# Optimization experiments

Measured on AMD Instinct MI355X. Metric: run time of the kernel, lower is better.

The kernel has to match this reference:

```python
import jax, jax.numpy as jnp
import numpy as np

B, S, F = 2, 2048, 1024
H, D = 16, 64
INIT = 0.02


def setup_inputs() -> dict:
    key = jax.random.key(0)
    k1, k2, k3 = jax.random.split(key, 3)
    x = jax.random.normal(k1, (B, S, F), dtype=jnp.float32)
    w_attn = jax.random.normal(k2, (F, 3 * F), dtype=jnp.float32) * INIT
    b_attn = jnp.zeros((3 * F,), dtype=jnp.float32)
    w_proj = jax.random.normal(k3, (F, F), dtype=jnp.float32) * INIT
    b_proj = jnp.zeros((F,), dtype=jnp.float32)
    return {"x": x, "w_attn": w_attn, "b_attn": b_attn, "w_proj": w_proj, "b_proj": b_proj}


def reference(x, w_attn, b_attn, w_proj, b_proj):
    # c_attn: [..., S, F] -> [..., S, 3F]
    qkv = jnp.einsum('bsf,fe->bse', x, w_attn) + b_attn
    q, k, v = jnp.split(qkv, 3, axis=-1)
    # split heads: [..., S, F] -> [..., S, H, D]
    q = q.reshape(q.shape[:-1] + (H, D))
    k = k.reshape(k.shape[:-1] + (H, D))
    v = v.reshape(v.shape[:-1] + (H, D))
    q = q / jnp.sqrt(jnp.asarray(D, dtype=q.dtype))
    # scores: [..., H, Sq, Sk]
    scores = jnp.einsum('bqhd,bkhd->bhqk', q, k)
    seq = x.shape[-2]
    causal = jnp.tril(jnp.ones((seq, seq), dtype=bool))  # [Sq, Sk]
    big_neg = jnp.finfo(scores.dtype).min
    scores = jnp.where(causal, scores, big_neg)
    weights = jax.nn.softmax(scores, axis=-1)
    z = jnp.einsum('bhqk,bkhd->bqhd', weights, v)
    merged = z.reshape(z.shape[:-2] + (F,))
    out = jnp.einsum('bsf,fe->bse', merged, w_proj) + b_proj
    return out
```

## Files before the change

### kernel.cpp

```cpp
#include <hip/hip_runtime.h>

#define B_ 2
#define S_ 2048
#define F_ 1024
#define H_ 16
#define D_ 64

typedef __bf16 bf16x8 __attribute__((ext_vector_type(8)));
typedef float f32x4 __attribute__((ext_vector_type(4)));
typedef float f32x16 __attribute__((ext_vector_type(16)));

union U8 { unsigned int u[4]; bf16x8 v; };

__device__ __forceinline__ unsigned short f2bf(float f) {
    union { float f; unsigned int u; } v;
    v.f = f;
    unsigned int r = v.u + 0x7fffu + ((v.u >> 16) & 1u);
    return (unsigned short)(r >> 16);
}

__device__ __forceinline__ unsigned int cvtpk_bf16(float lo, float hi) {
    unsigned int r;
    asm("v_cvt_pk_bf16_f32 %0, %1, %2" : "=v"(r) : "v"(lo), "v"(hi));
    return r;
}

__device__ __forceinline__ float xhalf_sum(float x) {
    return x + __shfl_xor(x, 32);
}

__device__ __forceinline__ void gload16(const unsigned short* g, unsigned short* l) {
    __builtin_amdgcn_global_load_lds(
        (const __attribute__((address_space(1))) unsigned int*)g,
        (__attribute__((address_space(3))) unsigned int*)l,
        16, 0, 0);
}

__global__ __launch_bounds__(256) void prep_kernel(const float* __restrict__ x, unsigned short* __restrict__ xb,
                                                   const float* __restrict__ wa, unsigned short* __restrict__ wat,
                                                   const float* __restrict__ wp, unsigned short* __restrict__ wpt) {
    __shared__ float t[32][33];
    int bid = blockIdx.x, tid = threadIdx.x;
    if (bid < 4096) {
        int i = bid * 256 + tid;
        float4 v = reinterpret_cast<const float4*>(x)[i];
        ushort4 o;
        o.x = f2bf(v.x); o.y = f2bf(v.y); o.z = f2bf(v.z); o.w = f2bf(v.w);
        reinterpret_cast<ushort4*>(xb)[i] = o;
        return;
    }
    const float* in;
    unsigned short* out;
    int R, C, bx, by;
    if (bid < 7168) {
        int loc = bid - 4096;
        bx = loc % 96; by = loc / 96;
        in = wa; out = wat; R = 1024; C = 3072;
    } else {
        int loc = bid - 7168;
        bx = loc & 31; by = loc >> 5;
        in = wp; out = wpt; R = 1024; C = 1024;
    }
    int tx = tid & 31, ty = tid >> 5;
    int r0 = by << 5, c0 = bx << 5;
#pragma unroll
    for (int kk = 0; kk < 4; ++kk)
        t[ty + 8 * kk][tx] = in[(size_t)(r0 + ty + 8 * kk) * C + c0 + tx];
    __syncthreads();
#pragma unroll
    for (int kk = 0; kk < 4; ++kk)
        out[(size_t)(c0 + ty + 8 * kk) * R + r0 + tx] = f2bf(t[tx][ty + 8 * kk]);
}

__global__ __launch_bounds__(512, 2) void gemm_qkv(const unsigned short* __restrict__ A,
                                                   const unsigned short* __restrict__ Bt,
                                                   const float* __restrict__ bias,
                                                   unsigned short* __restrict__ qo,
                                                   unsigned short* __restrict__ ko,
                                                   unsigned short* __restrict__ vo) {
    __shared__ __align__(16) unsigned short lds[65536];
    const int K = 1024;
    int bid = blockIdx.x;
    int swz = (bid & 7) * 24 + (bid >> 3);
    int by = swz / 12, bx = swz % 12;
    int m0 = by << 8, n0 = bx << 8;
    int tid = threadIdx.x;
    int wid = tid >> 6, l = tid & 63, lg = l >> 4, lr = l & 15;
    int wr = wid >> 2, wc = wid & 3;
    f32x4 acc[8][4] = {};

    int g0 = tid, g1 = tid + 512;
    int r0 = g0 >> 3, p0 = g0 & 7;
    int r1 = g1 >> 3, p1 = g1 & 7;
    int c0 = (p0 ^ (r0 & 7)) << 3;
    int c1 = (p1 ^ (r1 & 7)) << 3;

    int xr = (lr & 7) << 3;
    int csw0 = (lg * 8) ^ xr;
    int csw1 = (32 + lg * 8) ^ xr;

    const unsigned short* A0 = A + (size_t)(m0 + r0) * K + c0;
    const unsigned short* A1 = A + (size_t)(m0 + r1) * K + c1;
    const unsigned short* A2 = A + (size_t)(m0 + 128 + r0) * K + c0;
    const unsigned short* A3 = A + (size_t)(m0 + 128 + r1) * K + c1;
    const unsigned short* B0 = Bt + (size_t)(n0 + r0) * K + c0;
    const unsigned short* B1 = Bt + (size_t)(n0 + r1) * K + c1;
    const unsigned short* B2 = Bt + (size_t)(n0 + 128 + r0) * K + c0;
    const unsigned short* B3 = Bt + (size_t)(n0 + 128 + r1) * K + c1;

    gload16(A0, &lds[g0 * 8]);
    gload16(A1, &lds[g1 * 8]);
    gload16(A2, &lds[8192 + g0 * 8]);
    gload16(A3, &lds[8192 + g1 * 8]);
    gload16(B0, &lds[16384 + g0 * 8]);
    gload16(B1, &lds[16384 + g1 * 8]);
    gload16(B2, &lds[24576 + g0 * 8]);
    gload16(B3, &lds[24576 + g1 * 8]);
    __syncthreads();

    for (int t = 0; t < 16; ++t) {
        int bo = (t & 1) * 32768;
        if (t < 15) {
            int no = ((t + 1) & 1) * 32768;
            int t64 = (t + 1) * 64;
            gload16(A0 + t64, &lds[no + g0 * 8]);
            gload16(A1 + t64, &lds[no + g1 * 8]);
            gload16(A2 + t64, &lds[no + 8192 + g0 * 8]);
            gload16(A3 + t64, &lds[no + 8192 + g1 * 8]);
            gload16(B0 + t64, &lds[no + 16384 + g0 * 8]);
            gload16(B1 + t64, &lds[no + 16384 + g1 * 8]);
            gload16(B2 + t64, &lds[no + 24576 + g0 * 8]);
            gload16(B3 + t64, &lds[no + 24576 + g1 * 8]);
        }
        bf16x8 Bf[8];
#pragma unroll
        for (int ni = 0; ni < 4; ++ni) {
            int rowB = wc * 64 + ni * 16 + lr;
            int ba = bo + 16384 + (rowB >> 7) * 8192 + (rowB & 127) * 64;
            Bf[ni * 2]     = *reinterpret_cast<const bf16x8*>(&lds[ba + csw0]);
            Bf[ni * 2 + 1] = *reinterpret_cast<const bf16x8*>(&lds[ba + csw1]);
        }
#pragma unroll
        for (int mi = 0; mi < 8; ++mi) {
            int aa = bo + wr * 8192 + (mi * 16 + lr) * 64;
            bf16x8 a0 = *reinterpret_cast<const bf16x8*>(&lds[aa + csw0]);
            bf16x8 a1 = *reinterpret_cast<const bf16x8*>(&lds[aa + csw1]);
#pragma unroll
            for (int ni = 0; ni < 4; ++ni) {
                acc[mi][ni] = __builtin_amdgcn_mfma_f32_16x16x32_bf16(a0, Bf[ni * 2], acc[mi][ni], 0, 0, 0);
                acc[mi][ni] = __builtin_amdgcn_mfma_f32_16x16x32_bf16(a1, Bf[ni * 2 + 1], acc[mi][ni], 0, 0, 0);
            }
        }
        __syncthreads();
    }

#pragma unroll
    for (int mi = 0; mi < 8; ++mi) {
#pragma unroll
        for (int ni = 0; ni < 4; ++ni) {
            int col = n0 + wc * 64 + ni * 16 + lr;
            float bv = bias[col];
            int part = col >> 10, cc = col & 1023, h = cc >> 6, d = cc & 63;
            int row0 = m0 + wr * 128 + mi * 16 + (lg << 2);
            int bb = row0 >> 11, s0 = row0 & 2047;
            int bh = bb * H_ + h;
            if (part == 2) {
                int jt = s0 >> 5, db = d >> 5, kf2 = (s0 >> 4) & 1, hi2 = (s0 >> 3) & 1;
                int ll = (d & 31) | (hi2 << 5), e0 = s0 & 7;
                ushort4 pk;
                unsigned short* p = reinterpret_cast<unsigned short*>(&pk);
#pragma unroll
                for (int r = 0; r < 4; ++r) p[r] = f2bf(acc[mi][ni][r] + bv);
                *reinterpret_cast<ushort4*>(
                    &vo[(size_t)((((bh * 64 + jt) * 2 + db) * 2 + kf2)) * 512 + ll * 8 + e0]) = pk;
            } else {
                unsigned short* dst = part == 0 ? qo : ko;
                float scale = part == 0 ? 0.125f * 1.44269504f : 1.0f;
                int t2 = s0 >> 5, kf2 = d >> 4, e = d & 7;
                int lbase = ((d >> 3) & 1) << 5;
                size_t fb = (size_t)((bh * 64 + t2) * 4 + kf2) * 512 + e;
#pragma unroll
                for (int r = 0; r < 4; ++r) {
                    float vv = (acc[mi][ni][r] + bv) * scale;
                    dst[fb + (size_t)((((s0 + r) & 31) | lbase)) * 8] = f2bf(vv);
                }
            }
        }
    }
}

__global__ __launch_bounds__(256) void gemm_proj(const unsigned short* __restrict__ A,
                                                 const unsigned short* __restrict__ Bt,
                                                 const float* __restrict__ bias,
                                                 float* __restrict__ out) {
    __shared__ __align__(16) unsigned short As[2 * 128 * 32];
    __shared__ __align__(16) unsigned short Bs[2 * 128 * 32];
    const int K = 1024, NT = 32;
    int m0 = blockIdx.y << 7, n0 = blockIdx.x << 7;
    int tid = threadIdx.x;
    int w = tid >> 6, l = tid & 63, lg = l >> 4, lr = l & 15;
    int wm = (w >> 1) << 6, wn = (w & 1) << 6;
    f32x4 acc[4][4] = {};

    int sr = tid >> 2, sc = (tid & 3) << 3;
    const unsigned short* Ab = A + (size_t)(m0 + sr) * K + sc;
    const unsigned short* Bb = Bt + (size_t)(n0 + sr) * K + sc;
    const size_t half = (size_t)64 * K;

    gload16(Ab, &As[tid * 8]);
    gload16(Ab + half, &As[2048 + tid * 8]);
    gload16(Bb, &Bs[tid * 8]);
    gload16(Bb + half, &Bs[2048 + tid * 8]);
    __syncthreads();

    for (int t = 0; t < NT; ++t) {
        int cur = (t & 1) * 4096;
        if (t + 1 < NT) {
            int nxt = ((t + 1) & 1) * 4096;
            int ko2 = (t + 1) * 32;
            gload16(Ab + ko2, &As[nxt + tid * 8]);
            gload16(Ab + ko2 + half, &As[nxt + 2048 + tid * 8]);
            gload16(Bb + ko2, &Bs[nxt + tid * 8]);
            gload16(Bb + ko2 + half, &Bs[nxt + 2048 + tid * 8]);
        }
        bf16x8 af[4], bfr[4];
#pragma unroll
        for (int mi = 0; mi < 4; ++mi)
            af[mi] = *reinterpret_cast<const bf16x8*>(&As[cur + (wm + mi * 16 + lr) * 32 + (lg << 3)]);
#pragma unroll
        for (int ni = 0; ni < 4; ++ni)
            bfr[ni] = *reinterpret_cast<const bf16x8*>(&Bs[cur + (wn + ni * 16 + lr) * 32 + (lg << 3)]);
#pragma unroll
        for (int mi = 0; mi < 4; ++mi)
#pragma unroll
            for (int ni = 0; ni < 4; ++ni)
                acc[mi][ni] = __builtin_amdgcn_mfma_f32_16x16x32_bf16(af[mi], bfr[ni], acc[mi][ni], 0, 0, 0);
        __syncthreads();
    }
#pragma unroll
    for (int mi = 0; mi < 4; ++mi) {
#pragma unroll
        for (int ni = 0; ni < 4; ++ni) {
            int col = n0 + wn + ni * 16 + lr;
            float bv = bias[col];
#pragma unroll
            for (int r = 0; r < 4; ++r) {
                int row = m0 + wm + mi * 16 + (lg << 2) + r;
                out[(size_t)row * F_ + col] = acc[mi][ni][r] + bv;
            }
        }
    }
}

__device__ __forceinline__ void attn_tile32(
    const unsigned short* __restrict__ k, const unsigned short* __restrict__ v,
    int bh, int jt, bool pref, bool diag, int qcol, int hi, size_t lofs,
    const bf16x8 (&qf)[4], bf16x8 (&kcur)[4], bf16x8 (&knxt)[4],
    float &lsum, f32x16 &ot0, f32x16 &ot1)
{
    bf16x8 vf[4];
    const unsigned short* vp = v + (size_t)(bh * 64 + jt) * 2048 + lofs;
#pragma unroll
    for (int i = 0; i < 4; ++i)
        vf[i] = *reinterpret_cast<const bf16x8*>(vp + i * 512);
    if (pref) {
        const unsigned short* kp = k + (size_t)(bh * 64 + jt + 1) * 2048 + lofs;
#pragma unroll
        for (int kf = 0; kf < 4; ++kf)
            knxt[kf] = *reinterpret_cast<const bf16x8*>(kp + kf * 512);
    }

    f32x16 st = {};
#pragma unroll
    for (int kf = 0; kf < 4; ++kf)
        st = __builtin_amdgcn_mfma_f32_32x32x16_bf16(kcur[kf], qf[kf], st, 0, 0, 0);

    if (diag) {
        int qmh = qcol - 4 * hi;
#pragma unroll
        for (int r = 0; r < 16; ++r) {
            const int kbase = (r & 3) + 8 * (r >> 2);
            st[r] = (kbase > qmh) ? -1e30f : st[r];
        }
    }

    float ps = 0.f;
#pragma unroll
    for (int r = 0; r < 16; ++r) { st[r] = exp2f(st[r]); ps += st[r]; }
    lsum += ps;

    U8 pa0, pa1;
#pragma unroll
    for (int f = 0; f < 2; ++f) {
        unsigned int a0 = cvtpk_bf16(st[f * 8 + 0], st[f * 8 + 1]);
        unsigned int b0 = cvtpk_bf16(st[f * 8 + 4], st[f * 8 + 5]);
        asm("v_permlane32_swap_b32 %0, %1" : "+v"(a0), "+v"(b0));
        unsigned int a1 = cvtpk_bf16(st[f * 8 + 2], st[f * 8 + 3]);
        unsigned int b1 = cvtpk_bf16(st[f * 8 + 6], st[f * 8 + 7]);
        asm("v_permlane32_swap_b32 %0, %1" : "+v"(a1), "+v"(b1));
        U8& pa = f ? pa1 : pa0;
        pa.u[0] = a0; pa.u[1] = a1; pa.u[2] = b0; pa.u[3] = b1;
    }

    ot0 = __builtin_amdgcn_mfma_f32_32x32x16_bf16(vf[0], pa0.v, ot0, 0, 0, 0);
    ot0 = __builtin_amdgcn_mfma_f32_32x32x16_bf16(vf[1], pa1.v, ot0, 0, 0, 0);
    ot1 = __builtin_amdgcn_mfma_f32_32x32x16_bf16(vf[2], pa0.v, ot1, 0, 0, 0);
    ot1 = __builtin_amdgcn_mfma_f32_32x32x16_bf16(vf[3], pa1.v, ot1, 0, 0, 0);
}

__global__ __launch_bounds__(256, 3) void attn_kernel(const unsigned short* __restrict__ q,
                                                      const unsigned short* __restrict__ k,
                                                      const unsigned short* __restrict__ v,
                                                      unsigned short* __restrict__ z) {
    __shared__ __align__(16) float mbuf[3][64][36];
    int bh = blockIdx.x;
    int qt = gridDim.y - 1 - blockIdx.y;
    int q0 = qt << 5;
    int tid = threadIdx.x, w = tid >> 6, l = tid & 63;
    int qcol = l & 31, hi = l >> 5;
    size_t lofs = (size_t)l * 8;

    bf16x8 qf[4];
    {
        const unsigned short* qp = q + (size_t)(bh * 64 + qt) * 2048 + lofs;
#pragma unroll
        for (int kf = 0; kf < 4; ++kf)
            qf[kf] = *reinterpret_cast<const bf16x8*>(qp + kf * 512);
    }

    f32x16 ot0 = {}, ot1 = {};
    float lsum = 0.f;

    int ntk = qt + 1;
    int bs = ntk >> 2, rem = ntk & 3;
    int cnt = bs + ((w >= 4 - rem) ? 1 : 0);
    int start = bs * w + ((w - (4 - rem)) > 0 ? (w - (4 - rem)) : 0);
    int end = start + cnt;

    if (cnt > 0) {
        bf16x8 kA[4], kB[4];
        const unsigned short* kp = k + (size_t)(bh * 64 + start) * 2048 + lofs;
#pragma unroll
        for (int kf = 0; kf < 4; ++kf)
            kA[kf] = *reinterpret_cast<const bf16x8*>(kp + kf * 512);

        int jt = start;
        for (;;) {
            attn_tile32(k, v, bh, jt, jt + 1 < end, jt == qt, qcol, hi, lofs,
                        qf, kA, kB, lsum, ot0, ot1);
            if (++jt >= end) break;
            attn_tile32(k, v, bh, jt, jt + 1 < end, jt == qt, qcol, hi, lofs,
                        qf, kB, kA, lsum, ot0, ot1);
            if (++jt >= end) break;
        }
    }

    lsum = xhalf_sum(lsum);

    if (w) {
        float* row = mbuf[w - 1][l];
        row[0] = lsum;
        *reinterpret_cast<f32x16*>(&row[4]) = ot0;
        *reinterpret_cast<f32x16*>(&row[20]) = ot1;
    }
    __syncthreads();
    if (w == 0) {
#pragma unroll
        for (int i = 0; i < 3; ++i) {
            lsum += mbuf[i][l][0];
            f32x16 t0 = *reinterpret_cast<const f32x16*>(&mbuf[i][l][4]);
            f32x16 t1 = *reinterpret_cast<const f32x16*>(&mbuf[i][l][20]);
            ot0 += t0;
            ot1 += t1;
        }

        float inv = 1.0f / lsum;
        int b = bh >> 4, h = bh & 15;
        size_t zrow = ((size_t)(b * S_ + q0 + qcol)) * F_ + h * D_;
#pragma unroll
        for (int db = 0; db < 2; ++db) {
#pragma unroll
            for (int rq = 0; rq < 4; ++rq) {
                ushort4 pk;
                unsigned short* pp = reinterpret_cast<unsigned short*>(&pk);
#pragma unroll
                for (int i = 0; i < 4; ++i) {
                    float val = (db == 0 ? ot0[rq * 4 + i] : ot1[rq * 4 + i]) * inv;
                    pp[i] = f2bf(val);
                }
                *reinterpret_cast<ushort4*>(&z[zrow + db * 32 + rq * 8 + hi * 4]) = pk;
            }
        }
    }
}

extern "C" void kernel_launch(void* const* d_in, const int* in_sizes, int n_in,
                              void* d_out, int out_size, void* d_ws, size_t ws_size,
                              hipStream_t stream) {
    const float* x      = (const float*)d_in[0];
    const float* w_attn = (const float*)d_in[1];
    const float* b_attn = (const float*)d_in[2];
    const float* w_proj = (const float*)d_in[3];
    const float* b_proj = (const float*)d_in[4];
    float* out = (float*)d_out;
    char* ws = (char*)d_ws;

    unsigned short* xb   = (unsigned short*)(ws);
    unsigned short* wa_t = (unsigned short*)(ws + 8388608);
    unsigned short* wp_t = (unsigned short*)(ws + 14680064);
    unsigned short* qb   = (unsigned short*)(ws + 16777216);
    unsigned short* kb   = (unsigned short*)(ws + 25165824);
    unsigned short* vb   = (unsigned short*)(ws + 33554432);
    unsigned short* zb   = xb;

    prep_kernel<<<8192, 256, 0, stream>>>(x, xb, w_attn, wa_t, w_proj, wp_t);
    gemm_qkv<<<192, 512, 0, stream>>>(xb, wa_t, b_attn, qb, kb, vb);
    attn_kernel<<<dim3(32, 64), 256, 0, stream>>>(qb, kb, vb, zb);
    gemm_proj<<<dim3(8, 32), 256, 0, stream>>>(zb, wp_t, b_proj, out);
}
```

Baseline: 105.3 us.

## Software-pipeline attention loop: issue next tile's QK MFMA before current softmax/PV

Splits the per-tile attention step into a QK-score phase and a softmax+PV phase, then reorders the loop so the next tile's QK matmul and loads are issued before the current tile's softmax and PV. The intent is to overlap MFMA score computation with exp/convert/permlane work and hide load latency. It keeps two score accumulators and two V fragment sets live at once, which raises register pressure and could reduce occupancy. The diagonal mask is applied only to the final tile, which holds because that tile is the only one that can equal qt.

```diff
diff --git a/kernel.cpp b/kernel.cpp
--- a/kernel.cpp
+++ b/kernel.cpp
@@ -252,29 +252,33 @@
     }
 }
 
-__device__ __forceinline__ void attn_tile32(
+__device__ __forceinline__ void qk_phase(
     const unsigned short* __restrict__ k, const unsigned short* __restrict__ v,
-    int bh, int jt, bool pref, bool diag, int qcol, int hi, size_t lofs,
-    const bf16x8 (&qf)[4], bf16x8 (&kcur)[4], bf16x8 (&knxt)[4],
+    int bh, int jt, bool prefK, size_t lofs,
+    const bf16x8 (&qf)[4], bf16x8 (&kcur)[4], bf16x8 (&knxt)[4], bf16x8 (&vf)[4],
+    f32x16 &st)
+{
+    const unsigned short* vp = v + (size_t)(bh * 64 + jt) * 2048 + lofs;
+#pragma unroll
+    for (int i = 0; i < 4; ++i)
+        vf[i] = *reinterpret_cast<const bf16x8*>(vp + i * 512);
+    if (prefK) {
+        const unsigned short* kp = k + (size_t)(bh * 64 + jt + 1) * 2048 + lofs;
+#pragma unroll
+        for (int kf = 0; kf < 4; ++kf)
+            knxt[kf] = *reinterpret_cast<const bf16x8*>(kp + kf * 512);
+    }
+    st = f32x16{};
+#pragma unroll
+    for (int kf = 0; kf < 4; ++kf)
+        st = __builtin_amdgcn_mfma_f32_32x32x16_bf16(kcur[kf], qf[kf], st, 0, 0, 0);
+}
+
+__device__ __forceinline__ void sm_pv(
+    f32x16 &st, bool diag, int qcol, int hi,
+    const bf16x8 (&vf)[4],
     float &lsum, f32x16 &ot0, f32x16 &ot1)
 {
-    bf16x8 vf[4];
-    const unsigned short* vp = v + (size_t)(bh * 64 + jt) * 2048 + lofs;
-#pragma unroll
-    for (int i = 0; i < 4; ++i)
-        vf[i] = *reinterpret_cast<const bf16x8*>(vp + i * 512);
-    if (pref) {
-        const unsigned short* kp = k + (size_t)(bh * 64 + jt + 1) * 2048 + lofs;
-#pragma unroll
-        for (int kf = 0; kf < 4; ++kf)
-            knxt[kf] = *reinterpret_cast<const bf16x8*>(kp + kf * 512);
-    }
-
-    f32x16 st = {};
-#pragma unroll
-    for (int kf = 0; kf < 4; ++kf)
-        st = __builtin_amdgcn_mfma_f32_32x32x16_bf16(kcur[kf], qf[kf], st, 0, 0, 0);
-
     if (diag) {
         int qmh = qcol - 4 * hi;
 #pragma unroll
@@ -283,7 +287,6 @@
             st[r] = (kbase > qmh) ? -1e30f : st[r];
         }
     }
-
     float ps = 0.f;
 #pragma unroll
     for (int r = 0; r < 16; ++r) { st[r] = exp2f(st[r]); ps += st[r]; }
@@ -338,20 +341,25 @@
     int end = start + cnt;
 
     if (cnt > 0) {
-        bf16x8 kA[4], kB[4];
+        bf16x8 kA[4], kB[4], vA[4], vB[4];
+        f32x16 stA, stB;
         const unsigned short* kp = k + (size_t)(bh * 64 + start) * 2048 + lofs;
 #pragma unroll
         for (int kf = 0; kf < 4; ++kf)
             kA[kf] = *reinterpret_cast<const bf16x8*>(kp + kf * 512);
 
-        int jt = start;
+        qk_phase(k, v, bh, start, start + 1 < end, lofs, qf, kA, kB, vA, stA);
+
+        int jt = start + 1;
         for (;;) {
-            attn_tile32(k, v, bh, jt, jt + 1 < end, jt == qt, qcol, hi, lofs,
-                        qf, kA, kB, lsum, ot0, ot1);
-            if (++jt >= end) break;
-            attn_tile32(k, v, bh, jt, jt + 1 < end, jt == qt, qcol, hi, lofs,
-                        qf, kB, kA, lsum, ot0, ot1);
-            if (++jt >= end) break;
+            if (jt >= end) { sm_pv(stA, end - 1 == qt, qcol, hi, vA, lsum, ot0, ot1); break; }
+            qk_phase(k, v, bh, jt, jt + 1 < end, lofs, qf, kB, kA, vB, stB);
+            sm_pv(stA, false, qcol, hi, vA, lsum, ot0, ot1);
+            ++jt;
+            if (jt >= end) { sm_pv(stB, end - 1 == qt, qcol, hi, vB, lsum, ot0, ot1); break; }
+            qk_phase(k, v, bh, jt, jt + 1 < end, lofs, qf, kA, kB, vA, stA);
+            sm_pv(stB, false, qcol, hi, vB, lsum, ot0, ot1);
+            ++jt;
         }
     }
 
```

Result: slower. 172.1 us (+63.5%).

## Deepen proj GEMM K-tile to 64 with XOR-swizzled LDS layout

Applied to the files above, without the earlier changes.

The output projection GEMM now stages 128x64 K-slices instead of 128x32, which halves the number of main-loop iterations and barriers. Global-to-LDS column chunks are XOR-swizzled by row, and the fragment reads apply the matching swizzle to avoid LDS bank conflicts on the wider rows. This doubles the LDS footprint to 64 KB per block and adds register pressure from eight B fragments, which may reduce occupancy.

```diff
diff --git a/kernel.cpp b/kernel.cpp
--- a/kernel.cpp
+++ b/kernel.cpp
@@ -193,48 +193,80 @@
                                                  const unsigned short* __restrict__ Bt,
                                                  const float* __restrict__ bias,
                                                  float* __restrict__ out) {
-    __shared__ __align__(16) unsigned short As[2 * 128 * 32];
-    __shared__ __align__(16) unsigned short Bs[2 * 128 * 32];
-    const int K = 1024, NT = 32;
+    __shared__ __align__(16) unsigned short As[2 * 128 * 64];
+    __shared__ __align__(16) unsigned short Bs[2 * 128 * 64];
+    const int K = 1024, NT = 16;
     int m0 = blockIdx.y << 7, n0 = blockIdx.x << 7;
     int tid = threadIdx.x;
     int w = tid >> 6, l = tid & 63, lg = l >> 4, lr = l & 15;
     int wm = (w >> 1) << 6, wn = (w & 1) << 6;
     f32x4 acc[4][4] = {};
 
-    int sr = tid >> 2, sc = (tid & 3) << 3;
-    const unsigned short* Ab = A + (size_t)(m0 + sr) * K + sc;
-    const unsigned short* Bb = Bt + (size_t)(n0 + sr) * K + sc;
-    const size_t half = (size_t)64 * K;
-
-    gload16(Ab, &As[tid * 8]);
-    gload16(Ab + half, &As[2048 + tid * 8]);
-    gload16(Bb, &Bs[tid * 8]);
-    gload16(Bb + half, &Bs[2048 + tid * 8]);
+    int g0 = tid, g1 = tid + 256, g2 = tid + 512, g3 = tid + 768;
+    int r0 = g0 >> 3, p0 = g0 & 7;
+    int r1 = g1 >> 3, p1 = g1 & 7;
+    int r2 = g2 >> 3, p2 = g2 & 7;
+    int r3 = g3 >> 3, p3 = g3 & 7;
+    int c0 = (p0 ^ (r0 & 7)) << 3;
+    int c1 = (p1 ^ (r1 & 7)) << 3;
+    int c2 = (p2 ^ (r2 & 7)) << 3;
+    int c3 = (p3 ^ (r3 & 7)) << 3;
+
+    int xr = (lr & 7) << 3;
+    int csw0 = (lg * 8) ^ xr;
+    int csw1 = (32 + lg * 8) ^ xr;
+
+    const unsigned short* A0 = A + (size_t)(m0 + r0) * K + c0;
+    const unsigned short* A1 = A + (size_t)(m0 + r1) * K + c1;
+    const unsigned short* A2 = A + (size_t)(m0 + r2) * K + c2;
+    const unsigned short* A3 = A + (size_t)(m0 + r3) * K + c3;
+    const unsigned short* B0 = Bt + (size_t)(n0 + r0) * K + c0;
+    const unsigned short* B1 = Bt + (size_t)(n0 + r1) * K + c1;
+    const unsigned short* B2 = Bt + (size_t)(n0 + r2) * K + c2;
+    const unsigned short* B3 = Bt + (size_t)(n0 + r3) * K + c3;
+
+    gload16(A0, &As[g0 * 8]);
+    gload16(A1, &As[g1 * 8]);
+    gload16(A2, &As[g2 * 8]);
+    gload16(A3, &As[g3 * 8]);
+    gload16(B0, &Bs[g0 * 8]);
+    gload16(B1, &Bs[g1 * 8]);
+    gload16(B2, &Bs[g2 * 8]);
+    gload16(B3, &Bs[g3 * 8]);
     __syncthreads();
 
     for (int t = 0; t < NT; ++t) {
-        int cur = (t & 1) * 4096;
+        int cur = (t & 1) * 8192;
         if (t + 1 < NT) {
-            int nxt = ((t + 1) & 1) * 4096;
-            int ko2 = (t + 1) * 32;
-            gload16(Ab + ko2, &As[nxt + tid * 8]);
-            gload16(Ab + ko2 + half, &As[nxt + 2048 + tid * 8]);
-            gload16(Bb + ko2, &Bs[nxt + tid * 8]);
-            gload16(Bb + ko2 + half, &Bs[nxt + 2048 + tid * 8]);
-        }
-        bf16x8 af[4], bfr[4];
-#pragma unroll
-        for (int mi = 0; mi < 4; ++mi)
-            af[mi] = *reinterpret_cast<const bf16x8*>(&As[cur + (wm + mi * 16 + lr) * 32 + (lg << 3)]);
-#pragma unroll
-        for (int ni = 0; ni < 4; ++ni)
-            bfr[ni] = *reinterpret_cast<const bf16x8*>(&Bs[cur + (wn + ni * 16 + lr) * 32 + (lg << 3)]);
-#pragma unroll
-        for (int mi = 0; mi < 4; ++mi)
-#pragma unroll
-            for (int ni = 0; ni < 4; ++ni)
-                acc[mi][ni] = __builtin_amdgcn_mfma_f32_16x16x32_bf16(af[mi], bfr[ni], acc[mi][ni], 0, 0, 0);
+            int nxt = ((t + 1) & 1) * 8192;
+            int ko2 = (t + 1) * 64;
+            gload16(A0 + ko2, &As[nxt + g0 * 8]);
+            gload16(A1 + ko2, &As[nxt + g1 * 8]);
+            gload16(A2 + ko2, &As[nxt + g2 * 8]);
+            gload16(A3 + ko2, &As[nxt + g3 * 8]);
+            gload16(B0 + ko2, &Bs[nxt + g0 * 8]);
+            gload16(B1 + ko2, &Bs[nxt + g1 * 8]);
+            gload16(B2 + ko2, &Bs[nxt + g2 * 8]);
+            gload16(B3 + ko2, &Bs[nxt + g3 * 8]);
+        }
+        bf16x8 Bf[8];
+#pragma unroll
+        for (int ni = 0; ni < 4; ++ni) {
+            int ba = cur + (wn + ni * 16 + lr) * 64;
+            Bf[ni * 2]     = *reinterpret_cast<const bf16x8*>(&Bs[ba + csw0]);
+            Bf[ni * 2 + 1] = *reinterpret_cast<const bf16x8*>(&Bs[ba + csw1]);
+        }
+#pragma unroll
+        for (int mi = 0; mi < 4; ++mi) {
+            int aa = cur + (wm + mi * 16 + lr) * 64;
+            bf16x8 a0 = *reinterpret_cast<const bf16x8*>(&As[aa + csw0]);
+            bf16x8 a1 = *reinterpret_cast<const bf16x8*>(&As[aa + csw1]);
+#pragma unroll
+            for (int ni = 0; ni < 4; ++ni) {
+                acc[mi][ni] = __builtin_amdgcn_mfma_f32_16x16x32_bf16(a0, Bf[ni * 2], acc[mi][ni], 0, 0, 0);
+                acc[mi][ni] = __builtin_amdgcn_mfma_f32_16x16x32_bf16(a1, Bf[ni * 2 + 1], acc[mi][ni], 0, 0, 0);
+            }
+        }
         __syncthreads();
     }
 #pragma unroll
```

After: 106.4 us. Within noise of the previous version (+1.1%).
